# Kernel tuning notes

Measured on AMD Instinct MI355X. Metric: run time of the kernel, lower is better.

Reference implementation:

```python
import jax, jax.numpy as jnp
import numpy as np

B, T, I, L, D, O = 256, 512, 512, 128, 4, 2
LN_EPS = 1e-5

def setup_inputs() -> dict:
    key = jax.random.key(0)
    ks = jax.random.split(key, 7)
    x = jax.random.normal(ks[0], (B, T, I), jnp.float32)
    # Xavier-ish scaling keeps the recurrence numerically tame
    W_in = jax.random.normal(ks[1], (L, D, I), jnp.float32) * (1.0 / np.sqrt(I))
    W_liquid = jax.random.normal(ks[2], (L, D, L), jnp.float32) * (1.0 / np.sqrt(L))
    W_gate = jax.random.normal(ks[3], (L, D), jnp.float32)
    b_liquid = jnp.zeros((L,), jnp.float32)
    W_out = jax.random.normal(ks[4], (O, L), jnp.float32) * (1.0 / np.sqrt(L))
    b_out = jnp.zeros((O,), jnp.float32)
    ln_w = jnp.ones((L,), jnp.float32)
    ln_b = jnp.zeros((L,), jnp.float32)
    leaky_rate = jnp.asarray(0.3, jnp.float32)
    return {"x": x, "W_in": W_in, "W_liquid": W_liquid, "W_gate": W_gate,
            "b_liquid": b_liquid, "W_out": W_out, "b_out": b_out,
            "ln_w": ln_w, "ln_b": ln_b, "leaky_rate": leaky_rate}

def reference(x, W_in, W_liquid, W_gate, b_liquid, W_out, b_out, ln_w, ln_b, leaky_rate):
    # Liquid dendritic RNN. Dropout is identity (eval mode).
    gate = jax.nn.sigmoid(W_gate)                                   # [L,D]
    # Input branch has no recurrent dependency -> batch it over all timesteps
    in_br = jax.nn.relu(jnp.einsum('ldi,bti->btld', W_in, x))       # [B,T,L,D]
    merged_in = jnp.einsum('btld,ld->btl', in_br, gate)             # [B,T,L]
    alpha = jax.nn.sigmoid(leaky_rate)

    def step(state, m_in_t):                                        # state [B,L]
        rec_br = jax.nn.relu(jnp.einsum('ldh,bh->bld', W_liquid, state))
        merged_rec = jnp.einsum('bld,ld->bl', rec_br, gate)
        li = m_in_t + merged_rec + b_liquid                         # [B,L]
        mu = jnp.mean(li, axis=-1, keepdims=True)
        var = jnp.var(li, axis=-1, keepdims=True)
        li = (li - mu) * jax.lax.rsqrt(var + LN_EPS) * ln_w + ln_b
        new_state = (1.0 - alpha) * state + alpha * jnp.tanh(li)
        return new_state, None

    state0 = jnp.zeros((x.shape[0], W_in.shape[0]), x.dtype)
    final_state, _ = jax.lax.scan(step, state0, jnp.swapaxes(merged_in, 0, 1))
    return final_state @ W_out.T + b_out                            # [B,O]
```

## Files before the change

### kernel.cpp

```cpp
#include <hip/hip_runtime.h>
#include <hip/hip_bf16.h>
#include <stdint.h>


typedef __bf16 bf16x8 __attribute__((ext_vector_type(8)));
typedef float f32x4_t __attribute__((ext_vector_type(4)));

__device__ inline unsigned short f2bf(float f) {
    union { float f; unsigned u; } v; v.f = f;
    unsigned r = v.u + 0x7fffu + ((v.u >> 16) & 1u);
    return (unsigned short)(r >> 16);
}

__device__ inline void lds_barrier() {
    asm volatile("s_waitcnt lgkmcnt(0)" ::: "memory");
    __builtin_amdgcn_s_barrier();
}

__global__ __launch_bounds__(256, 2)
void gemm_in_kernel(const float* __restrict__ x, const float* __restrict__ W_in,
                    const float* __restrict__ W_gate, float* __restrict__ mt)
{
    __shared__ unsigned short As[128 * 32];
    __shared__ unsigned short Bs[128 * 32];

    const int tid = threadIdx.x;
    const int m0 = blockIdx.y * 128;
    const int n0 = blockIdx.x * 128;
    const int lane = tid & 63;
    const int wid  = tid >> 6;
    const int wr = wid >> 1, wc = wid & 1;
    const int fr = lane & 15, fq = lane >> 4;

    f32x4_t acc[4][4];
    #pragma unroll
    for (int i = 0; i < 4; ++i)
        #pragma unroll
        for (int j = 0; j < 4; ++j)
            acc[i][j] = (f32x4_t){0.f, 0.f, 0.f, 0.f};

    for (int k0 = 0; k0 < 512; k0 += 32) {
        #pragma unroll
        for (int p = 0; p < 4; ++p) {
            int ch = tid + p * 256;
            int r  = ch >> 3;
            int c  = ch & 7;
            float4 va = *(const float4*)(x    + (size_t)(m0 + r) * 512 + k0 + c * 4);
            float4 vb = *(const float4*)(W_in + (size_t)(n0 + r) * 512 + k0 + c * 4);
            ushort4 ha, hb;
            ha.x = f2bf(va.x); ha.y = f2bf(va.y); ha.z = f2bf(va.z); ha.w = f2bf(va.w);
            hb.x = f2bf(vb.x); hb.y = f2bf(vb.y); hb.z = f2bf(vb.z); hb.w = f2bf(vb.w);
            *(ushort4*)(&As[r * 32 + c * 4]) = ha;
            *(ushort4*)(&Bs[r * 32 + c * 4]) = hb;
        }
        __syncthreads();

        bf16x8 af[4], bfr[4];
        #pragma unroll
        for (int mi = 0; mi < 4; ++mi)
            af[mi] = *(const bf16x8*)(&As[(wr * 64 + mi * 16 + fr) * 32 + fq * 8]);
        #pragma unroll
        for (int ni = 0; ni < 4; ++ni)
            bfr[ni] = *(const bf16x8*)(&Bs[(wc * 64 + ni * 16 + fr) * 32 + fq * 8]);

        #pragma unroll
        for (int mi = 0; mi < 4; ++mi)
            #pragma unroll
            for (int ni = 0; ni < 4; ++ni)
                acc[mi][ni] = __builtin_amdgcn_mfma_f32_16x16x32_bf16(
                                  af[mi], bfr[ni], acc[mi][ni], 0, 0, 0);
        __syncthreads();
    }

    float gv[4];
    #pragma unroll
    for (int ni = 0; ni < 4; ++ni) {
        int n = n0 + wc * 64 + ni * 16 + fr;
        gv[ni] = 1.f / (1.f + __expf(-W_gate[n]));
    }
    #pragma unroll
    for (int mi = 0; mi < 4; ++mi) {
        #pragma unroll
        for (int ni = 0; ni < 4; ++ni) {
            int n = n0 + wc * 64 + ni * 16 + fr;
            int l = n >> 2;
            #pragma unroll
            for (int j = 0; j < 4; ++j) {
                float v = acc[mi][ni][j];
                float r = fmaxf(v, 0.f) * gv[ni];
                r += __shfl_xor(r, 1);
                r += __shfl_xor(r, 2);
                if ((lane & 3) == 0) {
                    int row = m0 + wr * 64 + mi * 16 + fq * 4 + j;
                    int bb = row >> 9;
                    int tt = row & 511;
                    mt[(size_t)bb * 65536 + (size_t)l * 512 + tt] = r;
                }
            }
        }
    }
}

__global__ __launch_bounds__(512, 2)
void scan_kernel(const float* __restrict__ mt, const float* __restrict__ W_liq,
                 const float* __restrict__ W_gate, const float* __restrict__ b_liq,
                 const float* __restrict__ W_out, const float* __restrict__ b_out,
                 const float* __restrict__ ln_w, const float* __restrict__ ln_b,
                 const float* __restrict__ leaky, float* __restrict__ out)
{
    __shared__ __align__(16) unsigned short s_bf[128];
    __shared__ __align__(16) float red[16];
    __shared__ float s_final[128];

    const int tid  = threadIdx.x;
    const int b    = blockIdx.x;
    const int lane = tid & 63;
    const int w    = tid >> 6;
    const int fr   = lane & 15;
    const int fq   = lane >> 4;

    bf16x8 wfrag[4][4];
    #pragma unroll
    for (int mi = 0; mi < 4; ++mi) {
        const float* wrow = W_liq + (size_t)(w * 64 + mi * 16 + fr) * 128;
        #pragma unroll
        for (int kk = 0; kk < 4; ++kk) {
            float4 f0 = *(const float4*)(wrow + kk * 32 + fq * 8);
            float4 f1 = *(const float4*)(wrow + kk * 32 + fq * 8 + 4);
            union { unsigned short u[8]; bf16x8 v; } cv;
            cv.u[0] = f2bf(f0.x); cv.u[1] = f2bf(f0.y);
            cv.u[2] = f2bf(f0.z); cv.u[3] = f2bf(f0.w);
            cv.u[4] = f2bf(f1.x); cv.u[5] = f2bf(f1.y);
            cv.u[6] = f2bf(f1.z); cv.u[7] = f2bf(f1.w);
            wfrag[mi][kk] = cv.v;
        }
    }

    int   l_mi[4];
    float gv[4][4], blv[4], lwv[4], lbv[4];
    size_t midx[4];
    #pragma unroll
    for (int mi = 0; mi < 4; ++mi) {
        int l = w * 16 + mi * 4 + fq;
        l_mi[mi] = l;
        #pragma unroll
        for (int r = 0; r < 4; ++r)
            gv[mi][r] = 1.f / (1.f + __expf(-W_gate[l * 4 + r]));
        blv[mi] = b_liq[l];
        lwv[mi] = ln_w[l];
        lbv[mi] = ln_b[l];
        midx[mi] = (size_t)b * 65536 + (size_t)l * 512;
    }
    const float alpha = 1.f / (1.f + __expf(-leaky[0]));
    const float oma   = 1.f - alpha;

    float s_reg[4] = {0.f, 0.f, 0.f, 0.f};

    float4 cur4[4], nxt4[4];
    #pragma unroll
    for (int mi = 0; mi < 4; ++mi) cur4[mi] = *(const float4*)(mt + midx[mi]);
    #pragma unroll
    for (int mi = 0; mi < 4; ++mi) nxt4[mi] = *(const float4*)(mt + midx[mi] + 4);

    if (tid < 64) ((unsigned*)s_bf)[tid] = 0u;
    lds_barrier();

    const f32x4_t z = {0.f, 0.f, 0.f, 0.f};

    for (int ts = 0; ts < 512; ts += 4) {
        float4 ld4[4];
        if (ts < 504) {
            #pragma unroll
            for (int mi = 0; mi < 4; ++mi)
                ld4[mi] = *(const float4*)(mt + midx[mi] + ts + 8);
        }

        #pragma unroll
        for (int ph = 0; ph < 4; ++ph) {
            bf16x8 bfr[4];
            #pragma unroll
            for (int kk = 0; kk < 4; ++kk)
                bfr[kk] = *(const bf16x8*)(&s_bf[kk * 32 + fq * 8]);

            f32x4_t a0[4], a1[4];
            #pragma unroll
            for (int mi = 0; mi < 4; ++mi) {
                a0[mi] = __builtin_amdgcn_mfma_f32_16x16x32_bf16(wfrag[mi][0], bfr[0], z, 0, 0, 0);
                a1[mi] = __builtin_amdgcn_mfma_f32_16x16x32_bf16(wfrag[mi][2], bfr[2], z, 0, 0, 0);
            }
            #pragma unroll
            for (int mi = 0; mi < 4; ++mi) {
                a0[mi] = __builtin_amdgcn_mfma_f32_16x16x32_bf16(wfrag[mi][1], bfr[1], a0[mi], 0, 0, 0);
                a1[mi] = __builtin_amdgcn_mfma_f32_16x16x32_bf16(wfrag[mi][3], bfr[3], a1[mi], 0, 0, 0);
            }

            float li[4], v1 = 0.f, v2 = 0.f;
            #pragma unroll
            for (int mi = 0; mi < 4; ++mi) {
                f32x4_t s4 = a0[mi] + a1[mi];
                float mr = gv[mi][0] * fmaxf(s4[0], 0.f);
                mr = fmaf(gv[mi][1], fmaxf(s4[1], 0.f), mr);
                mr = fmaf(gv[mi][2], fmaxf(s4[2], 0.f), mr);
                mr = fmaf(gv[mi][3], fmaxf(s4[3], 0.f), mr);
                li[mi] = cur4[mi][ph] + mr + blv[mi];
                v1 += li[mi];
                v2 = fmaf(li[mi], li[mi], v2);
            }
            v1 += __shfl_xor(v1, 16);  v2 += __shfl_xor(v2, 16);
            v1 += __shfl_xor(v1, 32);  v2 += __shfl_xor(v2, 32);
            if (lane == 0) { red[w] = v1; red[8 + w] = v2; }
            lds_barrier();

            float4 ra = *(const float4*)&red[0], rb = *(const float4*)&red[4];
            float4 rc = *(const float4*)&red[8], rd = *(const float4*)&red[12];
            float S1 = ((ra.x + ra.y) + (ra.z + ra.w)) + ((rb.x + rb.y) + (rb.z + rb.w));
            float S2 = ((rc.x + rc.y) + (rc.z + rc.w)) + ((rd.x + rd.y) + (rd.z + rd.w));
            float mean = S1 * (1.f / 128.f);
            float var  = fmaf(-mean, mean, S2 * (1.f / 128.f));
            float rstd = rsqrtf(var + 1e-5f);

            #pragma unroll
            for (int mi = 0; mi < 4; ++mi) {
                float t1 = rstd * lwv[mi];
                float xn = fmaf(li[mi], t1, fmaf(-mean, t1, lbv[mi]));
                float e  = __expf(2.f * xn);
                float th = fmaf(-2.f, __builtin_amdgcn_rcpf(e + 1.f), 1.f);
                s_reg[mi] = fmaf(oma, s_reg[mi], alpha * th);
            }
            if (fr == 0) {
                #pragma unroll
                for (int mi = 0; mi < 4; ++mi)
                    s_bf[l_mi[mi]] = f2bf(s_reg[mi]);
            }
            lds_barrier();
        }

        #pragma unroll
        for (int mi = 0; mi < 4; ++mi) cur4[mi] = nxt4[mi];
        if (ts < 504) {
            #pragma unroll
            for (int mi = 0; mi < 4; ++mi) nxt4[mi] = ld4[mi];
        }
    }

    if (fr == 0) {
        #pragma unroll
        for (int mi = 0; mi < 4; ++mi) s_final[l_mi[mi]] = s_reg[mi];
    }
    __syncthreads();
    if (tid < 2) {
        float accO = b_out[tid];
        #pragma unroll
        for (int h = 0; h < 128; ++h)
            accO = fmaf(s_final[h], W_out[tid * 128 + h], accO);
        out[b * 2 + tid] = accO;
    }
}

extern "C" void kernel_launch(void* const* d_in, const int* in_sizes, int n_in,
                              void* d_out, int out_size, void* d_ws, size_t ws_size,
                              hipStream_t stream)
{
    const float* x      = (const float*)d_in[0];
    const float* W_in   = (const float*)d_in[1];
    const float* W_liq  = (const float*)d_in[2];
    const float* W_gate = (const float*)d_in[3];
    const float* b_liq  = (const float*)d_in[4];
    const float* W_out  = (const float*)d_in[5];
    const float* b_out  = (const float*)d_in[6];
    const float* ln_w   = (const float*)d_in[7];
    const float* ln_b   = (const float*)d_in[8];
    const float* leaky  = (const float*)d_in[9];
    float* out = (float*)d_out;
    float* mt  = (float*)d_ws;

    gemm_in_kernel<<<dim3(4, 1024), 256, 0, stream>>>(x, W_in, W_gate, mt);
    scan_kernel<<<256, 512, 0, stream>>>(mt, W_liq, W_gate, b_liq,
                                         W_out, b_out, ln_w, ln_b, leaky, out);
}
```

Measured before the change: 703.5 us.

## Fold gate into recurrent weights, move bias to input GEMM, split tanh across lanes

```diff
diff --git a/kernel.cpp b/kernel.cpp
--- a/kernel.cpp
+++ b/kernel.cpp
@@ -19,7 +19,8 @@
 
 __global__ __launch_bounds__(256, 2)
 void gemm_in_kernel(const float* __restrict__ x, const float* __restrict__ W_in,
-                    const float* __restrict__ W_gate, float* __restrict__ mt)
+                    const float* __restrict__ W_gate, const float* __restrict__ b_liq,
+                    float* __restrict__ mt)
 {
     __shared__ unsigned short As[128 * 32];
     __shared__ unsigned short Bs[128 * 32];
@@ -72,11 +73,12 @@
         __syncthreads();
     }
 
-    float gv[4];
+    float gv[4], blq[4];
     #pragma unroll
     for (int ni = 0; ni < 4; ++ni) {
         int n = n0 + wc * 64 + ni * 16 + fr;
-        gv[ni] = 1.f / (1.f + __expf(-W_gate[n]));
+        gv[ni]  = 1.f / (1.f + __expf(-W_gate[n]));
+        blq[ni] = b_liq[n >> 2];
     }
     #pragma unroll
     for (int mi = 0; mi < 4; ++mi) {
@@ -94,7 +96,7 @@
                     int row = m0 + wr * 64 + mi * 16 + fq * 4 + j;
                     int bb = row >> 9;
                     int tt = row & 511;
-                    mt[(size_t)bb * 65536 + (size_t)l * 512 + tt] = r;
+                    mt[(size_t)bb * 65536 + (size_t)l * 512 + tt] = r + blq[ni];
                 }
             }
         }
@@ -103,13 +105,13 @@
 
 __global__ __launch_bounds__(512, 2)
 void scan_kernel(const float* __restrict__ mt, const float* __restrict__ W_liq,
-                 const float* __restrict__ W_gate, const float* __restrict__ b_liq,
-                 const float* __restrict__ W_out, const float* __restrict__ b_out,
-                 const float* __restrict__ ln_w, const float* __restrict__ ln_b,
-                 const float* __restrict__ leaky, float* __restrict__ out)
+                 const float* __restrict__ W_gate, const float* __restrict__ W_out,
+                 const float* __restrict__ b_out, const float* __restrict__ ln_w,
+                 const float* __restrict__ ln_b, const float* __restrict__ leaky,
+                 float* __restrict__ out)
 {
     __shared__ __align__(16) unsigned short s_bf[128];
-    __shared__ __align__(16) float red[16];
+    __shared__ __align__(16) float red2[16];
     __shared__ float s_final[128];
 
     const int tid  = threadIdx.x;
@@ -122,39 +124,35 @@
     bf16x8 wfrag[4][4];
     #pragma unroll
     for (int mi = 0; mi < 4; ++mi) {
-        const float* wrow = W_liq + (size_t)(w * 64 + mi * 16 + fr) * 128;
+        const int n = w * 64 + mi * 16 + fr;
+        const float gn = 1.f / (1.f + __expf(-W_gate[n]));
+        const float* wrow = W_liq + (size_t)n * 128;
         #pragma unroll
         for (int kk = 0; kk < 4; ++kk) {
             float4 f0 = *(const float4*)(wrow + kk * 32 + fq * 8);
             float4 f1 = *(const float4*)(wrow + kk * 32 + fq * 8 + 4);
             union { unsigned short u[8]; bf16x8 v; } cv;
-            cv.u[0] = f2bf(f0.x); cv.u[1] = f2bf(f0.y);
-            cv.u[2] = f2bf(f0.z); cv.u[3] = f2bf(f0.w);
-            cv.u[4] = f2bf(f1.x); cv.u[5] = f2bf(f1.y);
-            cv.u[6] = f2bf(f1.z); cv.u[7] = f2bf(f1.w);
+            cv.u[0] = f2bf(gn * f0.x); cv.u[1] = f2bf(gn * f0.y);
+            cv.u[2] = f2bf(gn * f0.z); cv.u[3] = f2bf(gn * f0.w);
+            cv.u[4] = f2bf(gn * f1.x); cv.u[5] = f2bf(gn * f1.y);
+            cv.u[6] = f2bf(gn * f1.z); cv.u[7] = f2bf(gn * f1.w);
             wfrag[mi][kk] = cv.v;
         }
     }
 
-    int   l_mi[4];
-    float gv[4][4], blv[4], lwv[4], lbv[4];
     size_t midx[4];
     #pragma unroll
-    for (int mi = 0; mi < 4; ++mi) {
-        int l = w * 16 + mi * 4 + fq;
-        l_mi[mi] = l;
-        #pragma unroll
-        for (int r = 0; r < 4; ++r)
-            gv[mi][r] = 1.f / (1.f + __expf(-W_gate[l * 4 + r]));
-        blv[mi] = b_liq[l];
-        lwv[mi] = ln_w[l];
-        lbv[mi] = ln_b[l];
-        midx[mi] = (size_t)b * 65536 + (size_t)l * 512;
-    }
+    for (int mi = 0; mi < 4; ++mi)
+        midx[mi] = (size_t)b * 65536 + (size_t)(w * 16 + mi * 4 + fq) * 512;
+
+    const int mi_own = fr >> 2;
+    const int l_own  = w * 16 + mi_own * 4 + fq;
+    const float lw_o = ln_w[l_own];
+    const float lb_o = ln_b[l_own];
     const float alpha = 1.f / (1.f + __expf(-leaky[0]));
     const float oma   = 1.f - alpha;
 
-    float s_reg[4] = {0.f, 0.f, 0.f, 0.f};
+    float s_own = 0.f;
 
     float4 cur4[4], nxt4[4];
     #pragma unroll
@@ -198,40 +196,38 @@
             #pragma unroll
             for (int mi = 0; mi < 4; ++mi) {
                 f32x4_t s4 = a0[mi] + a1[mi];
-                float mr = gv[mi][0] * fmaxf(s4[0], 0.f);
-                mr = fmaf(gv[mi][1], fmaxf(s4[1], 0.f), mr);
-                mr = fmaf(gv[mi][2], fmaxf(s4[2], 0.f), mr);
-                mr = fmaf(gv[mi][3], fmaxf(s4[3], 0.f), mr);
-                li[mi] = cur4[mi][ph] + mr + blv[mi];
+                float mr = (fmaxf(s4[0], 0.f) + fmaxf(s4[1], 0.f))
+                         + (fmaxf(s4[2], 0.f) + fmaxf(s4[3], 0.f));
+                li[mi] = cur4[mi][ph] + mr;
                 v1 += li[mi];
                 v2 = fmaf(li[mi], li[mi], v2);
             }
             v1 += __shfl_xor(v1, 16);  v2 += __shfl_xor(v2, 16);
             v1 += __shfl_xor(v1, 32);  v2 += __shfl_xor(v2, 32);
-            if (lane == 0) { red[w] = v1; red[8 + w] = v2; }
+            if (lane == 0) { red2[2 * w] = v1; red2[2 * w + 1] = v2; }
             lds_barrier();
 
-            float4 ra = *(const float4*)&red[0], rb = *(const float4*)&red[4];
-            float4 rc = *(const float4*)&red[8], rd = *(const float4*)&red[12];
-            float S1 = ((ra.x + ra.y) + (ra.z + ra.w)) + ((rb.x + rb.y) + (rb.z + rb.w));
-            float S2 = ((rc.x + rc.y) + (rc.z + rc.w)) + ((rd.x + rd.y) + (rd.z + rd.w));
+            float4 r0 = *(const float4*)&red2[0],  r1 = *(const float4*)&red2[4];
+            float4 r2 = *(const float4*)&red2[8],  r3 = *(const float4*)&red2[12];
+            float S1 = ((r0.x + r0.z) + (r1.x + r1.z)) + ((r2.x + r2.z) + (r3.x + r3.z));
+            float S2 = ((r0.y + r0.w) + (r1.y + r1.w)) + ((r2.y + r2.w) + (r3.y + r3.w));
             float mean = S1 * (1.f / 128.f);
             float var  = fmaf(-mean, mean, S2 * (1.f / 128.f));
             float rstd = rsqrtf(var + 1e-5f);
 
-            #pragma unroll
-            for (int mi = 0; mi < 4; ++mi) {
-                float t1 = rstd * lwv[mi];
-                float xn = fmaf(li[mi], t1, fmaf(-mean, t1, lbv[mi]));
-                float e  = __expf(2.f * xn);
-                float th = fmaf(-2.f, __builtin_amdgcn_rcpf(e + 1.f), 1.f);
-                s_reg[mi] = fmaf(oma, s_reg[mi], alpha * th);
-            }
-            if (fr == 0) {
-                #pragma unroll
-                for (int mi = 0; mi < 4; ++mi)
-                    s_bf[l_mi[mi]] = f2bf(s_reg[mi]);
-            }
+            float li01 = (lane & 4) ? li[1] : li[0];
+            float li23 = (lane & 4) ? li[3] : li[2];
+            float li_o = (lane & 8) ? li23 : li01;
+
+            float t1 = rstd * lw_o;
+            float xn = fmaf(li_o, t1, fmaf(-mean, t1, lb_o));
+            float e  = __builtin_amdgcn_exp2f(xn * 2.8853900817779268f);
+            float th = fmaf(-2.f, __builtin_amdgcn_rcpf(e + 1.f), 1.f);
+            s_own = fmaf(oma, s_own, alpha * th);
+
+            unsigned cvt;
+            asm("v_cvt_pk_bf16_f32 %0, %1, %2" : "=v"(cvt) : "v"(s_own), "v"(0.f));
+            if ((fr & 3) == 0) s_bf[l_own] = (unsigned short)cvt;
             lds_barrier();
         }
 
@@ -243,10 +239,7 @@
         }
     }
 
-    if (fr == 0) {
-        #pragma unroll
-        for (int mi = 0; mi < 4; ++mi) s_final[l_mi[mi]] = s_reg[mi];
-    }
+    if ((fr & 3) == 0) s_final[l_own] = s_own;
     __syncthreads();
     if (tid < 2) {
         float accO = b_out[tid];
@@ -274,7 +267,7 @@
     float* out = (float*)d_out;
     float* mt  = (float*)d_ws;
 
-    gemm_in_kernel<<<dim3(4, 1024), 256, 0, stream>>>(x, W_in, W_gate, mt);
-    scan_kernel<<<256, 512, 0, stream>>>(mt, W_liq, W_gate, b_liq,
+    gemm_in_kernel<<<dim3(4, 1024), 256, 0, stream>>>(x, W_in, W_gate, b_liq, mt);
+    scan_kernel<<<256, 512, 0, stream>>>(mt, W_liq, W_gate,
                                          W_out, b_out, ln_w, ln_b, leaky, out);
 }
```

Result: faster. 684.4 us (-2.7%).
